# Performance work log

Hardware: AMD Instinct MI355X
Metric: run time of the kernel (lower is better)

The kernel has to match this reference:

```python
import jax, jax.numpy as jnp
import numpy as np

N = 20000      # nodes
E = 640000     # edges (avg degree 32)
IN = 32        # input_dim
HID = 256      # hidden_dim
H = 8          # num_heads
Dh = HID // H  # head_dim = 32
TD = 32        # time_dim
L = 3          # num_layers
OUT = 2


def setup_inputs() -> dict:
    key = jax.random.key(0)
    ks = jax.random.split(key, 20)
    def w(k, sh):
        return (jax.random.normal(k, sh, jnp.float32) * 0.05)
    return {
        "x": jax.random.normal(ks[0], (N, IN), jnp.float32),
        "timestamps": jax.random.uniform(ks[1], (N,), jnp.float32),
        "edge_index": jax.random.randint(ks[2], (2, E), 0, N, jnp.int32),
        "batch": jnp.zeros((N,), jnp.int32),
        "time_freq": jax.random.normal(ks[3], (TD // 2,), jnp.float32),
        "inW": w(ks[4], (IN, HID)), "inb": jnp.zeros((HID,), jnp.float32),
        "qW": w(ks[5], (L, HID + TD, HID)), "qb": jnp.zeros((L, HID), jnp.float32),
        "kW": w(ks[6], (L, HID + TD, HID)), "kb": jnp.zeros((L, HID), jnp.float32),
        "vW": w(ks[7], (L, HID, HID)), "vb": jnp.zeros((L, HID), jnp.float32),
        "oW": w(ks[8], (L, HID, HID)), "ob": jnp.zeros((L, HID), jnp.float32),
        "c1W": w(ks[9], (HID, HID // 2)), "c1b": jnp.zeros((HID // 2,), jnp.float32),
        "c2W": w(ks[10], (HID // 2, OUT)), "c2b": jnp.zeros((OUT,), jnp.float32),
    }


def reference(x, timestamps, time_freq, inW, inb, qW, qb, kW, kb, vW, vb,
              oW, ob, c1W, c1b, c2W, c2b, edge_index, batch):
    n = x.shape[0]
    src, dst = edge_index[0], edge_index[1]

    # Functional time encoding (node-level timestamps branch)
    t = (timestamps - timestamps.min()) / (timestamps.max() - timestamps.min() + 1e-8)
    wt = t[:, None] * time_freq[None, :]                      # [N, TD/2]
    tf = jnp.concatenate([jnp.cos(wt), jnp.sin(wt)], axis=-1)  # [N, TD]

    h = x @ inW + inb                                          # [N, HID]
    scale = 1.0 / np.sqrt(Dh).astype(np.float32)

    for l in range(L):
        xt = jnp.concatenate([h, tf], axis=-1)                 # [N, HID+TD]
        Q = (xt @ qW[l] + qb[l]).reshape(n, H, Dh)
        K = (xt @ kW[l] + kb[l]).reshape(n, H, Dh)
        V = (h @ vW[l] + vb[l]).reshape(n, H, Dh)

        # per-edge attention scores [E, H]
        scores = jnp.einsum('ehd,ehd->eh', Q[dst], K[src]) * scale

        # segment softmax over incoming edges of each dst node
        m = jax.ops.segment_max(scores, dst, num_segments=n)   # [N, H]
        e = jnp.exp(scores - m[dst])
        s = jax.ops.segment_sum(e, dst, num_segments=n)        # [N, H]
        att = e / s[dst]                                       # [E, H]

        msgs = att[..., None] * V[src]                         # [E, H, Dh]
        out = jax.ops.segment_sum(msgs, dst, num_segments=n)   # [N, H, Dh]
        out = out.reshape(n, HID) @ oW[l] + ob[l]
        h = jax.nn.elu(out)

    # global mean pool (single graph: batch all zeros)
    cnt = jax.ops.segment_sum(jnp.ones((n, 1), h.dtype), batch, num_segments=1)
    g = jax.ops.segment_sum(h, batch, num_segments=1) / jnp.maximum(cnt, 1.0)

    logits = jax.nn.relu(g @ c1W + c1b) @ c2W + c2b            # [1, OUT]
    return logits
```

## Files before the change

kernel.cpp:

```cpp
#include <hip/hip_runtime.h>
#include <math.h>

#define HID 256
#define TD 32
#define NL 3
#define C1DIM 128
#define OUTDIM 2
#define QKVW 768

using half8  = __attribute__((ext_vector_type(8))) _Float16;
using half2v = __attribute__((ext_vector_type(2))) _Float16;
using f32x4  = __attribute__((ext_vector_type(4))) float;

typedef __attribute__((address_space(1))) void gbl_void_t;
typedef __attribute__((address_space(3))) void lds_void_t;

__device__ __forceinline__ void load16_to_lds(const void* g, void* l) {
  __builtin_amdgcn_global_load_lds((const gbl_void_t*)g, (lds_void_t*)l, 16, 0, 0);
}

__device__ __forceinline__ float dot8(half8 a, half8 b) {
#if __has_builtin(__builtin_amdgcn_fdot2)
  union { half8 v; half2v h2[4]; } ua, ub;
  ua.v = a; ub.v = b;
  float acc = 0.f;
#pragma unroll
  for (int j = 0; j < 4; ++j) acc = __builtin_amdgcn_fdot2(ua.h2[j], ub.h2[j], acc, false);
  return acc;
#else
  float acc = 0.f;
#pragma unroll
  for (int j = 0; j < 8; ++j) acc += (float)a[j] * (float)b[j];
  return acc;
#endif
}

__global__ __launch_bounds__(1024) void k_tsmm(const float* __restrict__ ts,
                                               float* __restrict__ mmf,
                                               int* __restrict__ deg, int n) {
  int t = threadIdx.x;
  float lmin = INFINITY, lmax = -INFINITY;
  for (int i = t; i < n; i += 1024) {
    float v = ts[i];
    lmin = fminf(lmin, v);
    lmax = fmaxf(lmax, v);
    deg[i] = 0;
  }
#pragma unroll
  for (int off = 32; off >= 1; off >>= 1) {
    lmin = fminf(lmin, __shfl_xor(lmin, off));
    lmax = fmaxf(lmax, __shfl_xor(lmax, off));
  }
  __shared__ float wmin[16], wmax[16];
  int lane = t & 63, w = t >> 6;
  if (lane == 0) { wmin[w] = lmin; wmax[w] = lmax; }
  __syncthreads();
  if (t == 0) {
    float a = INFINITY, b = -INFINITY;
    for (int i = 0; i < 16; ++i) { a = fminf(a, wmin[i]); b = fmaxf(b, wmax[i]); }
    mmf[0] = a; mmf[1] = b;
  }
}

__global__ void k_enc(const float* __restrict__ ts, const float* __restrict__ freq,
                      const float* __restrict__ mmf, const float* __restrict__ x,
                      _Float16* __restrict__ tfh, _Float16* __restrict__ xh, int n) {
  int idx = blockIdx.x * blockDim.x + threadIdx.x;
  int nt = n * TD;
  if (idx < nt) {
    int node = idx >> 5, j = idx & 31;
    float t = (ts[node] - mmf[0]) / (mmf[1] - mmf[0] + 1e-8f);
    float w = t * freq[j & 15];
    tfh[idx] = (_Float16)((j < 16) ? cosf(w) : sinf(w));
  } else if (idx < nt + n * 32) {
    int i2 = idx - nt;
    xh[i2] = (_Float16)x[i2];
  }
}

__global__ void k_prep(const float* __restrict__ inW, const float* __restrict__ qW,
                       const float* __restrict__ kW, const float* __restrict__ vW,
                       const float* __restrict__ oW, const float* __restrict__ qb,
                       const float* __restrict__ kb, const float* __restrict__ vb,
                       _Float16* __restrict__ inWt, _Float16* __restrict__ qkvWt,
                       float* __restrict__ qkvb, _Float16* __restrict__ oWt) {
  int idx = blockIdx.x * blockDim.x + threadIdx.x;
  const int S0 = 32 * HID;
  const int KQ = HID + TD;
  const int S1 = NL * QKVW * KQ;
  const int S2 = NL * QKVW;
  const int S3 = NL * HID * HID;
  if (idx < S0) {
    int nrow = idx / 32, k = idx - nrow * 32;
    inWt[idx] = (_Float16)inW[k * HID + nrow];
  } else if ((idx -= S0) < S1) {
    int l = idx / (QKVW * KQ);
    int rem = idx - l * (QKVW * KQ);
    int nrow = rem / KQ;
    int k = rem - nrow * KQ;
    float v;
    if (nrow < 256)      v = qW[(size_t)l * KQ * HID + (size_t)k * HID + nrow];
    else if (nrow < 512) v = kW[(size_t)l * KQ * HID + (size_t)k * HID + (nrow - 256)];
    else                 v = (k < HID) ? vW[(size_t)l * HID * HID + (size_t)k * HID + (nrow - 512)] : 0.f;
    qkvWt[idx] = (_Float16)v;
  } else if ((idx -= S1) < S2) {
    int l = idx / QKVW;
    int j = idx - l * QKVW;
    float v;
    if (j < 256)      v = qb[l * HID + j];
    else if (j < 512) v = kb[l * HID + (j - 256)];
    else              v = vb[l * HID + (j - 512)];
    qkvb[idx] = v;
  } else if ((idx -= S2) < S3) {
    int l = idx / (HID * HID);
    int rem = idx - l * (HID * HID);
    int nrow = rem / HID;
    int k = rem - nrow * HID;
    oWt[idx] = (_Float16)oW[(size_t)l * HID * HID + (size_t)k * HID + nrow];
  }
}

__global__ void k_count(const int* __restrict__ dst, int* deg, int e) {
  int i = blockIdx.x * blockDim.x + threadIdx.x;
  if (i < e) atomicAdd(&deg[dst[i]], 1);
}

__global__ __launch_bounds__(256) void k_scan_part(const int* __restrict__ deg,
                                                   int* __restrict__ bsum, int n) {
  int t = threadIdx.x;
  int idx = blockIdx.x * 256 + t;
  int v = (idx < n) ? deg[idx] : 0;
  int lane = t & 63, w = t >> 6;
  int x = v;
#pragma unroll
  for (int off = 1; off < 64; off <<= 1) {
    int y = __shfl_up(x, off);
    if (lane >= off) x += y;
  }
  __shared__ int ws[4];
  if (lane == 63) ws[w] = x;
  __syncthreads();
  if (t == 0) bsum[blockIdx.x] = ws[0] + ws[1] + ws[2] + ws[3];
}

__global__ __launch_bounds__(64) void k_scan_mid(const int* __restrict__ bsum,
                                                 int* __restrict__ boff, int nb) {
  int lane = threadIdx.x;
  int carry = 0;
  for (int base = 0; base < nb; base += 64) {
    int i = base + lane;
    int v = (i < nb) ? bsum[i] : 0;
    int x = v;
#pragma unroll
    for (int off = 1; off < 64; off <<= 1) {
      int y = __shfl_up(x, off);
      if (lane >= off) x += y;
    }
    if (i < nb) boff[i] = carry + x - v;
    carry += __shfl(x, 63);
  }
}

__global__ __launch_bounds__(256) void k_scan_apply(const int* __restrict__ deg,
                                                    const int* __restrict__ boff,
                                                    int* __restrict__ row_ptr,
                                                    int* __restrict__ cursor, int n, int e) {
  int t = threadIdx.x;
  int idx = blockIdx.x * 256 + t;
  int v = (idx < n) ? deg[idx] : 0;
  int lane = t & 63, w = t >> 6;
  int x = v;
#pragma unroll
  for (int off = 1; off < 64; off <<= 1) {
    int y = __shfl_up(x, off);
    if (lane >= off) x += y;
  }
  __shared__ int ws[4];
  if (lane == 63) ws[w] = x;
  __syncthreads();
  int wpre = 0;
  for (int i = 0; i < w; ++i) wpre += ws[i];
  if (idx < n) {
    row_ptr[idx] = boff[blockIdx.x] + wpre + x - v;
    cursor[idx] = 0;
  }
  if (idx == 0) row_ptr[n] = e;
}

__global__ void k_scatter(const int* __restrict__ src, const int* __restrict__ dst,
                          const int* __restrict__ row_ptr, int* cursor,
                          int* __restrict__ colbuf, int e) {
  int i = blockIdx.x * blockDim.x + threadIdx.x;
  if (i >= e) return;
  int d = dst[i];
  int p = atomicAdd(&cursor[d], 1);
  colbuf[row_ptr[d] + p] = src[i];
}

__global__ __launch_bounds__(256) void k_gemm_f16(
    const _Float16* __restrict__ A1, int K1,
    const _Float16* __restrict__ A2, int K2,
    const _Float16* __restrict__ Bt,
    const float* __restrict__ bias,
    _Float16* __restrict__ C,
    int M, int Ncols, int Ktot, int act) {
  __shared__ half8 smem8[2 * 768];
  char* smem = (char*)smem8;
  const int tid = threadIdx.x;
  const int lane = tid & 63, wave = tid >> 6;
  const int wm = wave >> 1, wn = wave & 1;
  const int row0 = blockIdx.y * 128;
  const int col0 = blockIdx.x * 64;

  auto stage = [&](int buf, int k0) {
    char* sA = smem + buf * 12288;
    char* sB = sA + 8192;
#pragma unroll
    for (int i = 0; i < 2; ++i) {
      int kg = i * 2 + (wave >> 1);
      int row = (wave & 1) * 64 + lane;
      int grow = row0 + row; if (grow > M - 1) grow = M - 1;
      int k = k0 + kg * 8;
      const _Float16* src = (k < K1) ? (A1 + (size_t)grow * K1 + k)
                                     : (A2 + (size_t)grow * K2 + (k - K1));
      load16_to_lds(src, sA + (i * 256 + wave * 64) * 16);
    }
    {
      const _Float16* src = Bt + (size_t)(col0 + lane) * Ktot + k0 + wave * 8;
      load16_to_lds(src, sB + wave * 64 * 16);
    }
  };

  f32x4 acc[4][2];
#pragma unroll
  for (int mf = 0; mf < 4; ++mf)
#pragma unroll
    for (int nf = 0; nf < 2; ++nf) acc[mf][nf] = f32x4{0.f, 0.f, 0.f, 0.f};

  const int nsteps = Ktot >> 5;
  int cur = 0;
  stage(0, 0);
  __syncthreads();
  for (int st = 0; st < nsteps; ++st) {
    if (st + 1 < nsteps) stage(cur ^ 1, (st + 1) * 32);
    char* sA = smem + cur * 12288;
    char* sB = sA + 8192;
    half8 af[4], bf[2];
#pragma unroll
    for (int mf = 0; mf < 4; ++mf) {
      int slot = (lane >> 4) * 128 + wm * 64 + mf * 16 + (lane & 15);
      af[mf] = *(const half8*)(sA + slot * 16);
    }
#pragma unroll
    for (int nf = 0; nf < 2; ++nf) {
      int slot = (lane >> 4) * 64 + wn * 32 + nf * 16 + (lane & 15);
      bf[nf] = *(const half8*)(sB + slot * 16);
    }
#pragma unroll
    for (int mf = 0; mf < 4; ++mf)
#pragma unroll
      for (int nf = 0; nf < 2; ++nf)
        acc[mf][nf] = __builtin_amdgcn_mfma_f32_16x16x32_f16(af[mf], bf[nf], acc[mf][nf], 0, 0, 0);
    __syncthreads();
    cur ^= 1;
  }

  const int rbase = row0 + wm * 64 + (lane >> 4) * 4;
  const int cbase = col0 + wn * 32 + (lane & 15);
#pragma unroll
  for (int nf = 0; nf < 2; ++nf) {
    int col = cbase + nf * 16;
    float bv = bias[col];
#pragma unroll
    for (int mf = 0; mf < 4; ++mf) {
#pragma unroll
      for (int r = 0; r < 4; ++r) {
        int row = rbase + mf * 16 + r;
        if (row < M) {
          float v = acc[mf][nf][r] + bv;
          if (act == 1) v = (v > 0.f) ? v : expm1f(v);
          C[(size_t)row * Ncols + col] = (_Float16)v;
        }
      }
    }
  }
}

__global__ __launch_bounds__(256) void k_attn(const _Float16* __restrict__ QKV,
                                              const int* __restrict__ row_ptr,
                                              const int* __restrict__ colbuf,
                                              _Float16* __restrict__ out, int n) {
  __shared__ float sm_m[4][8], sm_s[4][8];
  __shared__ float sm_a[4][32][9];
  int tid = threadIdx.x;
  int g = tid >> 5, t32 = tid & 31;
  int nl = g >> 1, hf = g & 1;
  int node = blockIdx.x * 4 + nl;
  bool act = node < n;
  int beg = 0, end = 0;
  if (act) { beg = row_ptr[node]; end = row_ptr[node + 1]; }
  int mid = beg + ((end - beg + 1) >> 1);
  int lo = hf ? mid : beg;
  int hi = hf ? end : mid;
  int d = t32 * 8;
  const float scale = 0.17677669529663687f;
  half8 qh = {};
  if (act) {
    qh = *(const half8*)(QKV + (size_t)node * QKVW + d);
#pragma unroll
    for (int j = 0; j < 8; ++j) qh[j] = (_Float16)((float)qh[j] * scale);
  }
  float m = -INFINITY, s = 0.f;
  float a[8] = {0.f, 0.f, 0.f, 0.f, 0.f, 0.f, 0.f, 0.f};

  for (int i = lo; i < hi; i += 4) {
    half8 kk[4], vv[4];
#pragma unroll
    for (int j = 0; j < 4; ++j) {
      int ii = i + j; if (ii > hi - 1) ii = hi - 1;
      int sn = colbuf[ii];
      const _Float16* bq = QKV + (size_t)sn * QKVW + d;
      kk[j] = *(const half8*)(bq + 256);
      vv[j] = *(const half8*)(bq + 512);
    }
    float p[4];
#pragma unroll
    for (int j = 0; j < 4; ++j) p[j] = dot8(qh, kk[j]);
#pragma unroll
    for (int j = 0; j < 4; ++j) {
      p[j] += __shfl_xor(p[j], 1);
      p[j] += __shfl_xor(p[j], 2);
      if (i + j >= hi) p[j] = -INFINITY;
    }
#pragma unroll
    for (int j = 0; j < 4; ++j) {
      float sc = p[j];
      if (sc <= m) {
        float e2 = __expf(sc - m);
        s += e2;
#pragma unroll
        for (int q = 0; q < 8; ++q) a[q] = fmaf(e2, (float)vv[j][q], a[q]);
      } else {
        float f = __expf(m - sc);
        s = s * f + 1.f;
#pragma unroll
        for (int q = 0; q < 8; ++q) a[q] = fmaf(a[q], f, (float)vv[j][q]);
        m = sc;
      }
    }
  }

  if (hf == 1 && act) {
    if ((t32 & 3) == 0) { sm_m[nl][t32 >> 2] = m; sm_s[nl][t32 >> 2] = s; }
#pragma unroll
    for (int q = 0; q < 8; ++q) sm_a[nl][t32][q] = a[q];
  }
  __syncthreads();
  if (hf == 0 && act) {
    float m1 = sm_m[nl][t32 >> 2], s1 = sm_s[nl][t32 >> 2];
    float M = fmaxf(m, m1);
    float f0 = (s > 0.f) ? __expf(m - M) : 0.f;
    float f1 = (s1 > 0.f) ? __expf(m1 - M) : 0.f;
    float S = s * f0 + s1 * f1;
    float inv = (S > 0.f) ? (1.f / S) : 0.f;
    half8 o;
#pragma unroll
    for (int q = 0; q < 8; ++q) o[q] = (_Float16)((a[q] * f0 + sm_a[nl][t32][q] * f1) * inv);
    *(half8*)(out + (size_t)node * HID + d) = o;
  }
}

__global__ __launch_bounds__(256) void k_pool_partial(const _Float16* __restrict__ h,
                                                      float* __restrict__ partial, int n) {
  int b = blockIdx.x, t = threadIdx.x;
  float s = 0.f;
  for (int r = b; r < n; r += 256) s += (float)h[(size_t)r * HID + t];
  partial[b * HID + t] = s;
}

__global__ __launch_bounds__(256) void k_final(const float* __restrict__ partial,
                                               const float* __restrict__ c1W,
                                               const float* __restrict__ c1b,
                                               const float* __restrict__ c2W,
                                               const float* __restrict__ c2b,
                                               float* __restrict__ out, int n) {
  __shared__ float gl[HID];
  __shared__ float r1[C1DIM];
  int t = threadIdx.x;
  float s = 0.f;
  for (int b = 0; b < 256; b++) s += partial[b * HID + t];
  gl[t] = s / (float)n;
  __syncthreads();
  if (t < C1DIM) {
    float a = c1b[t];
    for (int k = 0; k < HID; k++) a += gl[k] * c1W[k * C1DIM + t];
    r1[t] = fmaxf(a, 0.f);
  }
  __syncthreads();
  if (t < OUTDIM) {
    float a = c2b[t];
    for (int k = 0; k < C1DIM; k++) a += r1[k] * c2W[k * OUTDIM + t];
    out[t] = a;
  }
}

extern "C" void kernel_launch(void* const* d_in, const int* in_sizes, int n_in,
                              void* d_out, int out_size, void* d_ws, size_t ws_size,
                              hipStream_t stream) {
  const float* x    = (const float*)d_in[0];
  const float* ts   = (const float*)d_in[1];
  const int*   ei   = (const int*)d_in[2];
  const float* freq = (const float*)d_in[4];
  const float* inW  = (const float*)d_in[5];
  const float* inb  = (const float*)d_in[6];
  const float* qW   = (const float*)d_in[7];
  const float* qb   = (const float*)d_in[8];
  const float* kW   = (const float*)d_in[9];
  const float* kb   = (const float*)d_in[10];
  const float* vW   = (const float*)d_in[11];
  const float* vb   = (const float*)d_in[12];
  const float* oW   = (const float*)d_in[13];
  const float* ob   = (const float*)d_in[14];
  const float* c1W  = (const float*)d_in[15];
  const float* c1b  = (const float*)d_in[16];
  const float* c2W  = (const float*)d_in[17];
  const float* c2b  = (const float*)d_in[18];

  int n = in_sizes[1];
  int e = in_sizes[2] / 2;
  const int* src = ei;
  const int* dst = ei + e;
  int nb = (n + 255) / 256;

  char* w = (char*)d_ws;
  size_t off = 0;
  auto alloc = [&](size_t bytes) -> char* {
    char* p = w + off;
    off = (off + bytes + 255) & ~(size_t)255;
    return p;
  };
  _Float16* tfh     = (_Float16*)alloc((size_t)n * TD * 2);
  _Float16* xh      = (_Float16*)alloc((size_t)n * 32 * 2);
  _Float16* h       = (_Float16*)alloc((size_t)n * HID * 2);
  _Float16* QKV     = (_Float16*)alloc((size_t)n * QKVW * 2);
  _Float16* ao      = (_Float16*)alloc((size_t)n * HID * 2);
  _Float16* inWt    = (_Float16*)alloc((size_t)32 * HID * 2);
  _Float16* qkvWt   = (_Float16*)alloc((size_t)NL * QKVW * (HID + TD) * 2);
  float*    qkvb    = (float*)alloc((size_t)NL * QKVW * 4);
  _Float16* oWt     = (_Float16*)alloc((size_t)NL * HID * HID * 2);
  int*      deg     = (int*)alloc((size_t)n * 4);
  int*      cursor  = (int*)alloc((size_t)n * 4);
  int*      row_ptr = (int*)alloc((size_t)(n + 1) * 4);
  int*      colbuf  = (int*)alloc((size_t)e * 4);
  int*      bsum    = (int*)alloc((size_t)nb * 4);
  int*      boff    = (int*)alloc((size_t)nb * 4);
  float*    partial = (float*)alloc((size_t)256 * HID * 4);
  float*    mmf     = (float*)alloc(256);

  int b256 = 256;
  hipLaunchKernelGGL(k_tsmm, dim3(1), dim3(1024), 0, stream, ts, mmf, deg, n);
  hipLaunchKernelGGL(k_enc, dim3((n * 64 + 255) / 256), dim3(b256), 0, stream,
                     ts, freq, mmf, x, tfh, xh, n);
  {
    int total = 32 * HID + NL * QKVW * (HID + TD) + NL * QKVW + NL * HID * HID;
    hipLaunchKernelGGL(k_prep, dim3((total + 255) / 256), dim3(b256), 0, stream,
                       inW, qW, kW, vW, oW, qb, kb, vb, inWt, qkvWt, qkvb, oWt);
  }
  hipLaunchKernelGGL(k_count, dim3((e + 255) / 256), dim3(b256), 0, stream, dst, deg, e);
  hipLaunchKernelGGL(k_scan_part, dim3(nb), dim3(b256), 0, stream, deg, bsum, n);
  hipLaunchKernelGGL(k_scan_mid, dim3(1), dim3(64), 0, stream, bsum, boff, nb);
  hipLaunchKernelGGL(k_scan_apply, dim3(nb), dim3(b256), 0, stream, deg, boff, row_ptr, cursor, n, e);
  hipLaunchKernelGGL(k_scatter, dim3((e + 255) / 256), dim3(b256), 0, stream, src, dst, row_ptr, cursor, colbuf, e);

  dim3 ggrid_h(HID / 64, (n + 127) / 128);
  dim3 ggrid_qkv(QKVW / 64, (n + 127) / 128);
  hipLaunchKernelGGL(k_gemm_f16, ggrid_h, dim3(b256), 0, stream,
                     xh, 32, xh, 32, inWt, inb, h, n, HID, 32, 0);

  for (int l = 0; l < NL; ++l) {
    const _Float16* qkvWtl = qkvWt + (size_t)l * QKVW * (HID + TD);
    const float*    qkvbl  = qkvb + (size_t)l * QKVW;
    const _Float16* oWtl   = oWt + (size_t)l * HID * HID;
    hipLaunchKernelGGL(k_gemm_f16, ggrid_qkv, dim3(b256), 0, stream,
                       h, HID, tfh, TD, qkvWtl, qkvbl, QKV, n, QKVW, HID + TD, 0);
    hipLaunchKernelGGL(k_attn, dim3((n + 3) / 4), dim3(b256), 0, stream,
                       QKV, row_ptr, colbuf, ao, n);
    hipLaunchKernelGGL(k_gemm_f16, ggrid_h, dim3(b256), 0, stream,
                       ao, HID, ao, HID, oWtl, ob + l * HID, h, n, HID, HID, 1);
  }

  hipLaunchKernelGGL(k_pool_partial, dim3(256), dim3(b256), 0, stream, h, partial, n);
  hipLaunchKernelGGL(k_final, dim3(1), dim3(b256), 0, stream, partial, c1W, c1b, c2W, c2b, (float*)d_out, n);
}
```

Before: 575.4 us.

## Store K/V head-major and split attention by head for gather locality

The QKV GEMM epilogue now writes Q row-major and K/V in a head-major [head][node][K|V 32] layout. The attention kernel is re-gridded so each block handles one head for 64 nodes, with 4 threads per node and no cross-half merge through LDS. The goal is for per-edge gathers to touch a compact per-head 128-byte K/V record, so that each head's 2.5 MB working set fits better in cache. The cost is scattered 2-byte stores in the GEMM epilogue and more serial edge iterations per thread.

```diff
diff --git a/kernel.cpp b/kernel.cpp
--- a/kernel.cpp
+++ b/kernel.cpp
@@ -9,6 +9,7 @@
 #define QKVW 768
 
 using half8  = __attribute__((ext_vector_type(8))) _Float16;
+using half4v = __attribute__((ext_vector_type(4))) _Float16;
 using half2v = __attribute__((ext_vector_type(2))) _Float16;
 using f32x4  = __attribute__((ext_vector_type(4))) float;
 
@@ -19,16 +20,14 @@
   __builtin_amdgcn_global_load_lds((const gbl_void_t*)g, (lds_void_t*)l, 16, 0, 0);
 }
 
-__device__ __forceinline__ float dot8(half8 a, half8 b) {
+__device__ __forceinline__ float dot8h(half8 a, half8 b, float acc) {
 #if __has_builtin(__builtin_amdgcn_fdot2)
   union { half8 v; half2v h2[4]; } ua, ub;
   ua.v = a; ub.v = b;
-  float acc = 0.f;
 #pragma unroll
   for (int j = 0; j < 4; ++j) acc = __builtin_amdgcn_fdot2(ua.h2[j], ub.h2[j], acc, false);
   return acc;
 #else
-  float acc = 0.f;
 #pragma unroll
   for (int j = 0; j < 8; ++j) acc += (float)a[j] * (float)b[j];
   return acc;
@@ -203,7 +202,9 @@
     const _Float16* __restrict__ Bt,
     const float* __restrict__ bias,
     _Float16* __restrict__ C,
-    int M, int Ncols, int Ktot, int act) {
+    _Float16* __restrict__ Qb,
+    _Float16* __restrict__ KV,
+    int M, int Ncols, int Ktot, int mode) {
   __shared__ half8 smem8[2 * 768];
   char* smem = (char*)smem8;
   const int tid = threadIdx.x;
@@ -271,103 +272,105 @@
   for (int nf = 0; nf < 2; ++nf) {
     int col = cbase + nf * 16;
     float bv = bias[col];
-#pragma unroll
-    for (int mf = 0; mf < 4; ++mf) {
-#pragma unroll
-      for (int r = 0; r < 4; ++r) {
-        int row = rbase + mf * 16 + r;
-        if (row < M) {
-          float v = acc[mf][nf][r] + bv;
-          if (act == 1) v = (v > 0.f) ? v : expm1f(v);
-          C[(size_t)row * Ncols + col] = (_Float16)v;
+    if (mode != 2) {
+#pragma unroll
+      for (int mf = 0; mf < 4; ++mf) {
+#pragma unroll
+        for (int r = 0; r < 4; ++r) {
+          int row = rbase + mf * 16 + r;
+          if (row < M) {
+            float v = acc[mf][nf][r] + bv;
+            if (mode == 1) v = (v > 0.f) ? v : expm1f(v);
+            C[(size_t)row * Ncols + col] = (_Float16)v;
+          }
         }
       }
-    }
-  }
-}
-
-__global__ __launch_bounds__(256) void k_attn(const _Float16* __restrict__ QKV,
+    } else {
+      bool isQ = col < 256;
+      int cc = col - 256;
+      int isV = cc >> 8;
+      int c2 = cc & 255;
+      int hh = c2 >> 5, dim = c2 & 31;
+      size_t kvoff = ((size_t)hh * M) * 64 + isV * 32 + dim;
+#pragma unroll
+      for (int mf = 0; mf < 4; ++mf) {
+#pragma unroll
+        for (int r = 0; r < 4; ++r) {
+          int row = rbase + mf * 16 + r;
+          if (row < M) {
+            float v = acc[mf][nf][r] + bv;
+            if (isQ) Qb[(size_t)row * HID + col] = (_Float16)v;
+            else     KV[kvoff + (size_t)row * 64] = (_Float16)v;
+          }
+        }
+      }
+    }
+  }
+}
+
+__global__ __launch_bounds__(256) void k_attn(const _Float16* __restrict__ Qb,
+                                              const _Float16* __restrict__ KV,
                                               const int* __restrict__ row_ptr,
                                               const int* __restrict__ colbuf,
                                               _Float16* __restrict__ out, int n) {
-  __shared__ float sm_m[4][8], sm_s[4][8];
-  __shared__ float sm_a[4][32][9];
-  int tid = threadIdx.x;
-  int g = tid >> 5, t32 = tid & 31;
-  int nl = g >> 1, hf = g & 1;
-  int node = blockIdx.x * 4 + nl;
-  bool act = node < n;
-  int beg = 0, end = 0;
-  if (act) { beg = row_ptr[node]; end = row_ptr[node + 1]; }
-  int mid = beg + ((end - beg + 1) >> 1);
-  int lo = hf ? mid : beg;
-  int hi = hf ? end : mid;
-  int d = t32 * 8;
+  int h = blockIdx.x & 7;
+  int node = (blockIdx.x >> 3) * 64 + (threadIdx.x >> 2);
+  if (node >= n) return;
+  int j = threadIdx.x & 3;
   const float scale = 0.17677669529663687f;
-  half8 qh = {};
-  if (act) {
-    qh = *(const half8*)(QKV + (size_t)node * QKVW + d);
-#pragma unroll
-    for (int j = 0; j < 8; ++j) qh[j] = (_Float16)((float)qh[j] * scale);
-  }
+  const _Float16* KVh = KV + ((size_t)h * n) * 64;
+
+  half8 qh = *(const half8*)(Qb + (size_t)node * HID + h * 32 + j * 8);
+  half8 qs;
+#pragma unroll
+  for (int q = 0; q < 8; ++q) qs[q] = (_Float16)((float)qh[q] * scale);
+
+  int beg = row_ptr[node], end = row_ptr[node + 1];
   float m = -INFINITY, s = 0.f;
   float a[8] = {0.f, 0.f, 0.f, 0.f, 0.f, 0.f, 0.f, 0.f};
 
-  for (int i = lo; i < hi; i += 4) {
+  for (int i = beg; i < end; i += 4) {
     half8 kk[4], vv[4];
 #pragma unroll
-    for (int j = 0; j < 4; ++j) {
-      int ii = i + j; if (ii > hi - 1) ii = hi - 1;
+    for (int t = 0; t < 4; ++t) {
+      int ii = i + t; if (ii > end - 1) ii = end - 1;
       int sn = colbuf[ii];
-      const _Float16* bq = QKV + (size_t)sn * QKVW + d;
-      kk[j] = *(const half8*)(bq + 256);
-      vv[j] = *(const half8*)(bq + 512);
+      const _Float16* b = KVh + ((size_t)sn) * 64 + j * 8;
+      kk[t] = *(const half8*)(b);
+      vv[t] = *(const half8*)(b + 32);
     }
     float p[4];
 #pragma unroll
-    for (int j = 0; j < 4; ++j) p[j] = dot8(qh, kk[j]);
-#pragma unroll
-    for (int j = 0; j < 4; ++j) {
-      p[j] += __shfl_xor(p[j], 1);
-      p[j] += __shfl_xor(p[j], 2);
-      if (i + j >= hi) p[j] = -INFINITY;
-    }
-#pragma unroll
-    for (int j = 0; j < 4; ++j) {
-      float sc = p[j];
-      if (sc <= m) {
-        float e2 = __expf(sc - m);
+    for (int t = 0; t < 4; ++t) p[t] = dot8h(qs, kk[t], 0.f);
+#pragma unroll
+    for (int t = 0; t < 4; ++t) {
+      p[t] += __shfl_xor(p[t], 1);
+      p[t] += __shfl_xor(p[t], 2);
+      if (i + t >= end) p[t] = -INFINITY;
+    }
+#pragma unroll
+    for (int t = 0; t < 4; ++t) {
+      float sc_ = p[t];
+      if (sc_ <= m) {
+        float e2 = __expf(sc_ - m);
         s += e2;
 #pragma unroll
-        for (int q = 0; q < 8; ++q) a[q] = fmaf(e2, (float)vv[j][q], a[q]);
+        for (int q = 0; q < 8; ++q) a[q] = fmaf(e2, (float)vv[t][q], a[q]);
       } else {
-        float f = __expf(m - sc);
+        float f = __expf(m - sc_);
         s = s * f + 1.f;
 #pragma unroll
-        for (int q = 0; q < 8; ++q) a[q] = fmaf(a[q], f, (float)vv[j][q]);
-        m = sc;
+        for (int q = 0; q < 8; ++q) a[q] = fmaf(a[q], f, (float)vv[t][q]);
+        m = sc_;
       }
     }
   }
 
-  if (hf == 1 && act) {
-    if ((t32 & 3) == 0) { sm_m[nl][t32 >> 2] = m; sm_s[nl][t32 >> 2] = s; }
-#pragma unroll
-    for (int q = 0; q < 8; ++q) sm_a[nl][t32][q] = a[q];
-  }
-  __syncthreads();
-  if (hf == 0 && act) {
-    float m1 = sm_m[nl][t32 >> 2], s1 = sm_s[nl][t32 >> 2];
-    float M = fmaxf(m, m1);
-    float f0 = (s > 0.f) ? __expf(m - M) : 0.f;
-    float f1 = (s1 > 0.f) ? __expf(m1 - M) : 0.f;
-    float S = s * f0 + s1 * f1;
-    float inv = (S > 0.f) ? (1.f / S) : 0.f;
-    half8 o;
-#pragma unroll
-    for (int q = 0; q < 8; ++q) o[q] = (_Float16)((a[q] * f0 + sm_a[nl][t32][q] * f1) * inv);
-    *(half8*)(out + (size_t)node * HID + d) = o;
-  }
+  float inv = (s > 0.f) ? (1.f / s) : 0.f;
+  half8 o;
+#pragma unroll
+  for (int q = 0; q < 8; ++q) o[q] = (_Float16)(a[q] * inv);
+  *(half8*)(out + (size_t)node * HID + h * 32 + j * 8) = o;
 }
 
 __global__ __launch_bounds__(256) void k_pool_partial(const _Float16* __restrict__ h,
@@ -442,7 +445,8 @@
   _Float16* tfh     = (_Float16*)alloc((size_t)n * TD * 2);
   _Float16* xh      = (_Float16*)alloc((size_t)n * 32 * 2);
   _Float16* h       = (_Float16*)alloc((size_t)n * HID * 2);
-  _Float16* QKV     = (_Float16*)alloc((size_t)n * QKVW * 2);
+  _Float16* Qbuf    = (_Float16*)alloc((size_t)n * HID * 2);
+  _Float16* KV      = (_Float16*)alloc((size_t)n * 512 * 2);
   _Float16* ao      = (_Float16*)alloc((size_t)n * HID * 2);
   _Float16* inWt    = (_Float16*)alloc((size_t)32 * HID * 2);
   _Float16* qkvWt   = (_Float16*)alloc((size_t)NL * QKVW * (HID + TD) * 2);
@@ -475,18 +479,22 @@
   dim3 ggrid_h(HID / 64, (n + 127) / 128);
   dim3 ggrid_qkv(QKVW / 64, (n + 127) / 128);
   hipLaunchKernelGGL(k_gemm_f16, ggrid_h, dim3(b256), 0, stream,
-                     xh, 32, xh, 32, inWt, inb, h, n, HID, 32, 0);
-
+                     xh, 32, xh, 32, inWt, inb, h, (_Float16*)nullptr, (_Float16*)nullptr,
+                     n, HID, 32, 0);
+
+  int nchunks = (n + 63) / 64;
   for (int l = 0; l < NL; ++l) {
     const _Float16* qkvWtl = qkvWt + (size_t)l * QKVW * (HID + TD);
     const float*    qkvbl  = qkvb + (size_t)l * QKVW;
     const _Float16* oWtl   = oWt + (size_t)l * HID * HID;
     hipLaunchKernelGGL(k_gemm_f16, ggrid_qkv, dim3(b256), 0, stream,
-                       h, HID, tfh, TD, qkvWtl, qkvbl, QKV, n, QKVW, HID + TD, 0);
-    hipLaunchKernelGGL(k_attn, dim3((n + 3) / 4), dim3(b256), 0, stream,
-                       QKV, row_ptr, colbuf, ao, n);
+                       h, HID, tfh, TD, qkvWtl, qkvbl, (_Float16*)nullptr, Qbuf, KV,
+                       n, QKVW, HID + TD, 2);
+    hipLaunchKernelGGL(k_attn, dim3(nchunks * 8), dim3(b256), 0, stream,
+                       Qbuf, KV, row_ptr, colbuf, ao, n);
     hipLaunchKernelGGL(k_gemm_f16, ggrid_h, dim3(b256), 0, stream,
-                       ao, HID, ao, HID, oWtl, ob + l * HID, h, n, HID, HID, 1);
+                       ao, HID, ao, HID, oWtl, ob + l * HID, h, (_Float16*)nullptr, (_Float16*)nullptr,
+                       n, HID, HID, 1);
   }
 
   hipLaunchKernelGGL(k_pool_partial, dim3(256), dim3(b256), 0, stream, h, partial, n);
```

New measurement: 481.1 us. 1.2x faster.
